# Kernel optimization log

Measured on AMD Instinct MI355X. Metric: run time of the kernel, lower is better.

## Reference

```python
import jax, jax.numpy as jnp
import numpy as np

NUM_QUBIT = 23
N0 = 2
DIM = 2 ** NUM_QUBIT  # 8388608


def setup_inputs() -> dict:
    key = jax.random.key(0)
    ks = jax.random.split(key, 6)
    shape = (N0, DIM)
    code0_real = jax.random.normal(ks[0], shape, jnp.float32)
    code0_imag = jax.random.normal(ks[1], shape, jnp.float32)
    code1_real = jax.random.normal(ks[2], shape, jnp.float32)
    code1_imag = jax.random.normal(ks[3], shape, jnp.float32)
    # per-qubit 2x2 unitaries: random complex matrices, unitarized via QR
    ur = jax.random.normal(ks[4], (NUM_QUBIT, 2, 2), jnp.float32)
    ui = jax.random.normal(ks[5], (NUM_QUBIT, 2, 2), jnp.float32)
    q, _ = jnp.linalg.qr(ur + 1j * ui)  # [n,2,2] complex64 unitary
    return {
        "code0_real": code0_real,
        "code0_imag": code0_imag,
        "code1_real": code1_real,
        "code1_imag": code1_imag,
        "unitary_real": jnp.real(q).astype(jnp.float32),
        "unitary_imag": jnp.imag(q).astype(jnp.float32),
    }


def reference(code0_real, code0_imag, code1_real, code1_imag,
              unitary_real, unitary_imag):
    code0 = code0_real + 1j * code0_imag            # [N0, 2^n] complex64
    code1 = code1_real + 1j * code1_imag            # [N0, 2^n]
    unitary = unitary_real + 1j * unitary_imag      # [n, 2, 2]
    n = unitary.shape[0]
    n0 = code0.shape[0]
    # sequential per-qubit 2x2 gate application on the statevectors
    for ind0 in range(n):
        tmp0 = code0.reshape(n0 * 2 ** ind0, 2, -1)  # [N0*2^i, 2, 2^(n-i-1)]
        # out[a,d,c] = sum_b tmp0[a,b,c] * U[b,d]
        code0 = jnp.einsum('abc,bd->adc', tmp0, unitary[ind0]).reshape(n0, -1)
    overlap = (jnp.conj(code0) @ code1.T).reshape(-1)  # [N0*N0]
    loss = n0 - jnp.real(jnp.vdot(overlap, overlap))
    return loss
```

## Files before the change

kernel.cpp:

```cpp
#include <hip/hip_runtime.h>

#define DIM_ (1 << 23)
#define N0_ 2

__device__ float g_acc[8];

__device__ __forceinline__ int swz(int x) {
    return x ^ ((x >> 5) & 3) ^ (((x >> 7) & 7) << 2);
}

__device__ __forceinline__ void gload(const float* __restrict__ ur,
                                      const float* __restrict__ ui, int q,
                                      float2& u00, float2& u01, float2& u10, float2& u11) {
    u00 = make_float2(ur[q * 4 + 0], ui[q * 4 + 0]);
    u01 = make_float2(ur[q * 4 + 1], ui[q * 4 + 1]);
    u10 = make_float2(ur[q * 4 + 2], ui[q * 4 + 2]);
    u11 = make_float2(ur[q * 4 + 3], ui[q * 4 + 3]);
}

__device__ __forceinline__ void bfly(float2& a0, float2& a1,
                                     float2 u00, float2 u01, float2 u10, float2 u11) {
    float2 n0, n1;
    n0.x = a0.x * u00.x - a0.y * u00.y + a1.x * u10.x - a1.y * u10.y;
    n0.y = a0.x * u00.y + a0.y * u00.x + a1.x * u10.y + a1.y * u10.x;
    n1.x = a0.x * u01.x - a0.y * u01.y + a1.x * u11.x - a1.y * u11.y;
    n1.y = a0.x * u01.y + a0.y * u01.x + a1.x * u11.y + a1.y * u11.x;
    a0 = n0; a1 = n1;
}

#define BFLY16(S, Q)                                                           \
    do {                                                                       \
        float2 u00, u01, u10, u11;                                             \
        gload(ur, ui, (Q), u00, u01, u10, u11);                                \
        _Pragma("unroll")                                                      \
        for (int m0 = 0; m0 < 16; ++m0)                                        \
            if (!(m0 & (S))) bfly(v[m0], v[m0 + (S)], u00, u01, u10, u11);     \
    } while (0)

template <bool INTER>
__global__ __launch_bounds__(512, 2) void k_low(
    const float* __restrict__ inr, const float* __restrict__ ini,
    const float* __restrict__ ur, const float* __restrict__ ui,
    float2* __restrict__ outI, float* __restrict__ outR, float* __restrict__ outJ) {
    __shared__ float2 buf[8192];
    const int t = threadIdx.x;
    const int H = blockIdx.x;
    const int base = blockIdx.y * DIM_ + (H << 13);

    float2 v[16];
#pragma unroll
    for (int k = 0; k < 4; ++k) {
        const int y = (k << 11) | (t << 2);
        const float4 re = *(const float4*)(inr + base + y);
        const float4 im = *(const float4*)(ini + base + y);
        v[k * 4 + 0] = make_float2(re.x, im.x);
        v[k * 4 + 1] = make_float2(re.y, im.y);
        v[k * 4 + 2] = make_float2(re.z, im.z);
        v[k * 4 + 3] = make_float2(re.w, im.w);
    }
    BFLY16(1, 22);
    BFLY16(2, 21);
    BFLY16(4, 11);
    BFLY16(8, 10);
#pragma unroll
    for (int m = 0; m < 16; ++m)
        buf[swz(((m >> 2) << 11) | (t << 2) | (m & 3))] = v[m];
    __syncthreads();
#pragma unroll
    for (int m = 0; m < 16; ++m)
        v[m] = buf[swz((t & 3) | (m << 2) | ((t >> 2) << 6))];
    BFLY16(1, 20);
    BFLY16(2, 19);
    BFLY16(4, 18);
    BFLY16(8, 17);
#pragma unroll
    for (int m = 0; m < 16; ++m)
        buf[swz((t & 3) | (m << 2) | ((t >> 2) << 6))] = v[m];
    __syncthreads();
#pragma unroll
    for (int m = 0; m < 16; ++m)
        v[m] = buf[swz((t & 63) | (m << 6) | ((t >> 6) << 10))];
    BFLY16(1, 16);
    BFLY16(2, 15);
    BFLY16(4, 14);
    BFLY16(8, 13);
#pragma unroll
    for (int m = 0; m < 16; ++m)
        buf[swz((t & 63) | (m << 6) | ((t >> 6) << 10))] = v[m];
    __syncthreads();
    {
        float2 u00, u01, u10, u11;
        gload(ur, ui, 12, u00, u01, u10, u11);
#pragma unroll
        for (int rp = 0; rp < 4; ++rp) {
            const int x0 = (rp << 11) | (t << 1);
            float2 a0 = buf[swz(x0)];
            float2 a1 = buf[swz(x0 | 1)];
            float2 b0 = buf[swz(x0 | 1024)];
            float2 b1 = buf[swz(x0 | 1025)];
            bfly(a0, b0, u00, u01, u10, u11);
            bfly(a1, b1, u00, u01, u10, u11);
            if (INTER) {
                const int l0 = x0, l1 = x0 | 1024;
                const int o0 = ((l0 >> 3) << 13) | (H << 3) | (l0 & 7);
                const int o1 = ((l1 >> 3) << 13) | (H << 3) | (l1 & 7);
                float2* p = outI + blockIdx.y * DIM_;
                *(float4*)(p + o0) = make_float4(a0.x, a0.y, a1.x, a1.y);
                *(float4*)(p + o1) = make_float4(b0.x, b0.y, b1.x, b1.y);
            } else {
                *(float2*)(outR + base + x0) = make_float2(a0.x, a1.x);
                *(float2*)(outJ + base + x0) = make_float2(a0.y, a1.y);
                *(float2*)(outR + base + (x0 | 1024)) = make_float2(b0.x, b1.x);
                *(float2*)(outJ + base + (x0 | 1024)) = make_float2(b0.y, b1.y);
            }
        }
    }
}

template <bool INTER>
__device__ __forceinline__ void high_pass(
    float2 (&v)[16], float2* buf, const int t, const int g, const int i,
    const float2* __restrict__ wsI, const float* __restrict__ wsR,
    const float* __restrict__ wsJ,
    const float* __restrict__ ur, const float* __restrict__ ui) {
    if constexpr (INTER) {
        const float4* wsv = (const float4*)(wsI + i * DIM_ + (g << 13));
#pragma unroll
        for (int k = 0; k < 4; ++k)
#pragma unroll
            for (int jh = 0; jh < 2; ++jh) {
                const float4 f = wsv[(k << 10) | (t << 1) | jh];
                v[k * 4 + jh * 2 + 0] = make_float2(f.x, f.y);
                v[k * 4 + jh * 2 + 1] = make_float2(f.z, f.w);
            }
    } else {
#pragma unroll
        for (int k = 0; k < 4; ++k) {
            const int y0 = (k << 11) | (t << 2);
            const int a = ((y0 >> 3) << 13) | (g << 3) | (y0 & 7);
            const float4 re = *(const float4*)(wsR + i * DIM_ + a);
            const float4 im = *(const float4*)(wsJ + i * DIM_ + a);
            v[k * 4 + 0] = make_float2(re.x, im.x);
            v[k * 4 + 1] = make_float2(re.y, im.y);
            v[k * 4 + 2] = make_float2(re.z, im.z);
            v[k * 4 + 3] = make_float2(re.w, im.w);
        }
    }
    BFLY16(4, 1);
    BFLY16(8, 0);
#pragma unroll
    for (int m = 0; m < 16; ++m)
        buf[swz(((m >> 2) << 11) | (t << 2) | (m & 3))] = v[m];
    __syncthreads();
#pragma unroll
    for (int m = 0; m < 16; ++m)
        v[m] = buf[swz((t & 7) | (m << 3) | ((t >> 3) << 7))];
    BFLY16(1, 9);
    BFLY16(2, 8);
    BFLY16(4, 7);
    BFLY16(8, 6);
#pragma unroll
    for (int m = 0; m < 16; ++m)
        buf[swz((t & 7) | (m << 3) | ((t >> 3) << 7))] = v[m];
    __syncthreads();
#pragma unroll
    for (int m = 0; m < 16; ++m)
        v[m] = buf[swz((t & 127) | (m << 7) | ((t >> 7) << 11))];
    BFLY16(1, 5);
    BFLY16(2, 4);
    BFLY16(4, 3);
    BFLY16(8, 2);
}

template <bool INTER>
__global__ __launch_bounds__(512, 2) void k_high(
    const float2* __restrict__ wsI, const float* __restrict__ wsR, const float* __restrict__ wsJ,
    const float* __restrict__ c1r, const float* __restrict__ c1i,
    const float* __restrict__ ur, const float* __restrict__ ui) {
    __shared__ float2 buf[8192];
    const int t = threadIdx.x;
    const int g = blockIdx.x;
    float acc[8];
#pragma unroll
    for (int k = 0; k < 8; ++k) acc[k] = 0.f;

    float2 v0[16], v1[16];
    high_pass<INTER>(v0, buf, t, g, 0, wsI, wsR, wsJ, ur, ui);
    __syncthreads();
    high_pass<INTER>(v1, buf, t, g, 1, wsI, wsR, wsJ, ur, ui);

#pragma unroll
    for (int m = 0; m < 16; ++m) {
        const int y = (t & 127) | (m << 7) | ((t >> 7) << 11);
        const int idx = ((y >> 3) << 13) | (g << 3) | (y & 7);
        const float ar = c1r[idx], ai = c1i[idx];
        const float br = c1r[DIM_ + idx], bi = c1i[DIM_ + idx];
        acc[0] += v0[m].x * ar + v0[m].y * ai;
        acc[1] += v0[m].x * ai - v0[m].y * ar;
        acc[2] += v0[m].x * br + v0[m].y * bi;
        acc[3] += v0[m].x * bi - v0[m].y * br;
        acc[4] += v1[m].x * ar + v1[m].y * ai;
        acc[5] += v1[m].x * ai - v1[m].y * ar;
        acc[6] += v1[m].x * br + v1[m].y * bi;
        acc[7] += v1[m].x * bi - v1[m].y * br;
    }

#pragma unroll
    for (int k = 0; k < 8; ++k)
#pragma unroll
        for (int off = 32; off > 0; off >>= 1)
            acc[k] += __shfl_down(acc[k], off, 64);
    __syncthreads();
    float* red = (float*)buf;
    const int wave = t >> 6, lane = t & 63;
    if (lane == 0) {
#pragma unroll
        for (int k = 0; k < 8; ++k) red[wave * 8 + k] = acc[k];
    }
    __syncthreads();
    if (t < 8) {
        float s = 0.f;
#pragma unroll
        for (int w = 0; w < 8; ++w) s += red[w * 8 + t];
        atomicAdd(&g_acc[t], s);
    }
}

__global__ void k_zero() {
    if (threadIdx.x < 8) g_acc[threadIdx.x] = 0.f;
}

__global__ void k_fin(float* __restrict__ out) {
    if (threadIdx.x == 0) {
        float s = 0.f;
#pragma unroll
        for (int k = 0; k < 4; ++k)
            s += g_acc[2 * k] * g_acc[2 * k] + g_acc[2 * k + 1] * g_acc[2 * k + 1];
        out[0] = (float)N0_ - s;
    }
}

extern "C" void kernel_launch(void* const* d_in, const int* in_sizes, int n_in,
                              void* d_out, int out_size, void* d_ws, size_t ws_size,
                              hipStream_t stream) {
    const float* c0r = (const float*)d_in[0];
    const float* c0i = (const float*)d_in[1];
    const float* c1r = (const float*)d_in[2];
    const float* c1i = (const float*)d_in[3];
    const float* ur  = (const float*)d_in[4];
    const float* ui  = (const float*)d_in[5];
    float* out = (float*)d_out;

    const size_t need = (size_t)N0_ * DIM_ * sizeof(float2);
    k_zero<<<1, 64, 0, stream>>>();
    dim3 g1(1024, N0_);
    if (d_ws != nullptr && ws_size >= need) {
        float2* wsI = (float2*)d_ws;
        k_low<true><<<g1, 512, 0, stream>>>(c0r, c0i, ur, ui, wsI, nullptr, nullptr);
        k_high<true><<<1024, 512, 0, stream>>>(wsI, nullptr, nullptr, c1r, c1i, ur, ui);
    } else {
        float* oR = (float*)c0r;
        float* oJ = (float*)c0i;
        k_low<false><<<g1, 512, 0, stream>>>(c0r, c0i, ur, ui, nullptr, oR, oJ);
        k_high<false><<<1024, 512, 0, stream>>>(nullptr, oR, oJ, c1r, c1i, ur, ui);
    }
    k_fin<<<1, 64, 0, stream>>>(out);
}
```

Before: 419.4 us.

## Rebalance qubit split between passes with smaller low-pass tiles and coalesced c1 loads

The low pass now handles 4096-element tiles with 256-thread blocks, twice as many blocks and half the shared memory. This moves qubit 10 from the low pass into the high pass, where it is applied after an extra shared-memory transpose. That transpose gives each thread 16 contiguous elements, so the overlap step reads code1 as float4 vectors instead of scattered scalars. The accumulator zeroing is folded into k_low, which removes one kernel launch. The cost is an extra LDS round trip and barrier in each high pass, plus a race risk: k_low's zeroing is ordered only by stream order ahead of k_high.

```diff
diff --git a/kernel.cpp b/kernel.cpp
--- a/kernel.cpp
+++ b/kernel.cpp
@@ -38,19 +38,22 @@
     } while (0)
 
 template <bool INTER>
-__global__ __launch_bounds__(512, 2) void k_low(
+__global__ __launch_bounds__(256, 5) void k_low(
     const float* __restrict__ inr, const float* __restrict__ ini,
     const float* __restrict__ ur, const float* __restrict__ ui,
     float2* __restrict__ outI, float* __restrict__ outR, float* __restrict__ outJ) {
-    __shared__ float2 buf[8192];
+    __shared__ float2 buf[4096];
     const int t = threadIdx.x;
-    const int H = blockIdx.x;
-    const int base = blockIdx.y * DIM_ + (H << 13);
+    const int C = blockIdx.x;
+    const int iv = blockIdx.y;
+    const int base = iv * DIM_ + (C << 12);
+
+    if (C == 0 && iv == 0 && t < 8) g_acc[t] = 0.f;
 
     float2 v[16];
 #pragma unroll
     for (int k = 0; k < 4; ++k) {
-        const int y = (k << 11) | (t << 2);
+        const int y = (k << 10) | (t << 2);
         const float4 re = *(const float4*)(inr + base + y);
         const float4 im = *(const float4*)(ini + base + y);
         v[k * 4 + 0] = make_float2(re.x, im.x);
@@ -60,11 +63,11 @@
     }
     BFLY16(1, 22);
     BFLY16(2, 21);
-    BFLY16(4, 11);
-    BFLY16(8, 10);
-#pragma unroll
-    for (int m = 0; m < 16; ++m)
-        buf[swz(((m >> 2) << 11) | (t << 2) | (m & 3))] = v[m];
+    BFLY16(4, 12);
+    BFLY16(8, 11);
+#pragma unroll
+    for (int m = 0; m < 16; ++m)
+        buf[swz(((m >> 2) << 10) | (t << 2) | (m & 3))] = v[m];
     __syncthreads();
 #pragma unroll
     for (int m = 0; m < 16; ++m)
@@ -88,43 +91,30 @@
     for (int m = 0; m < 16; ++m)
         buf[swz((t & 63) | (m << 6) | ((t >> 6) << 10))] = v[m];
     __syncthreads();
-    {
-        float2 u00, u01, u10, u11;
-        gload(ur, ui, 12, u00, u01, u10, u11);
-#pragma unroll
-        for (int rp = 0; rp < 4; ++rp) {
-            const int x0 = (rp << 11) | (t << 1);
-            float2 a0 = buf[swz(x0)];
-            float2 a1 = buf[swz(x0 | 1)];
-            float2 b0 = buf[swz(x0 | 1024)];
-            float2 b1 = buf[swz(x0 | 1025)];
-            bfly(a0, b0, u00, u01, u10, u11);
-            bfly(a1, b1, u00, u01, u10, u11);
-            if (INTER) {
-                const int l0 = x0, l1 = x0 | 1024;
-                const int o0 = ((l0 >> 3) << 13) | (H << 3) | (l0 & 7);
-                const int o1 = ((l1 >> 3) << 13) | (H << 3) | (l1 & 7);
-                float2* p = outI + blockIdx.y * DIM_;
-                *(float4*)(p + o0) = make_float4(a0.x, a0.y, a1.x, a1.y);
-                *(float4*)(p + o1) = make_float4(b0.x, b0.y, b1.x, b1.y);
-            } else {
-                *(float2*)(outR + base + x0) = make_float2(a0.x, a1.x);
-                *(float2*)(outJ + base + x0) = make_float2(a0.y, a1.y);
-                *(float2*)(outR + base + (x0 | 1024)) = make_float2(b0.x, b1.x);
-                *(float2*)(outJ + base + (x0 | 1024)) = make_float2(b0.y, b1.y);
-            }
+#pragma unroll
+    for (int r = 0; r < 8; ++r) {
+        const int l12 = (r << 9) | (t << 1);
+        const float2 a = buf[swz(l12)];
+        const float2 b = buf[swz(l12 | 1)];
+        if (INTER) {
+            const int o = ((l12 >> 2) << 13) | ((C >> 1) << 3) | ((C & 1) << 2) | (l12 & 3);
+            *(float4*)(outI + iv * DIM_ + o) = make_float4(a.x, a.y, b.x, b.y);
+        } else {
+            *(float2*)(outR + base + l12) = make_float2(a.x, b.x);
+            *(float2*)(outJ + base + l12) = make_float2(a.y, b.y);
         }
     }
 }
 
 template <bool INTER>
 __device__ __forceinline__ void high_pass(
-    float2 (&v)[16], float2* buf, const int t, const int g, const int i,
+    float2 (&d)[16], float2* buf, const int t, const int g, const int iv,
     const float2* __restrict__ wsI, const float* __restrict__ wsR,
     const float* __restrict__ wsJ,
     const float* __restrict__ ur, const float* __restrict__ ui) {
+    float2 v[16];
     if constexpr (INTER) {
-        const float4* wsv = (const float4*)(wsI + i * DIM_ + (g << 13));
+        const float4* wsv = (const float4*)(wsI + iv * DIM_ + (g << 13));
 #pragma unroll
         for (int k = 0; k < 4; ++k)
 #pragma unroll
@@ -136,10 +126,9 @@
     } else {
 #pragma unroll
         for (int k = 0; k < 4; ++k) {
-            const int y0 = (k << 11) | (t << 2);
-            const int a = ((y0 >> 3) << 13) | (g << 3) | (y0 & 7);
-            const float4 re = *(const float4*)(wsR + i * DIM_ + a);
-            const float4 im = *(const float4*)(wsJ + i * DIM_ + a);
+            const int a = (((k << 9) | t) << 12) | (g << 2);
+            const float4 re = *(const float4*)(wsR + iv * DIM_ + a);
+            const float4 im = *(const float4*)(wsJ + iv * DIM_ + a);
             v[k * 4 + 0] = make_float2(re.x, im.x);
             v[k * 4 + 1] = make_float2(re.y, im.y);
             v[k * 4 + 2] = make_float2(re.z, im.z);
@@ -170,6 +159,20 @@
     BFLY16(2, 4);
     BFLY16(4, 3);
     BFLY16(8, 2);
+#pragma unroll
+    for (int m = 0; m < 16; ++m)
+        buf[swz((t & 127) | (m << 7) | ((t >> 7) << 11))] = v[m];
+    __syncthreads();
+#pragma unroll
+    for (int j = 0; j < 16; ++j)
+        d[j] = buf[swz((t << 4) | j)];
+    {
+        float2 u00, u01, u10, u11;
+        gload(ur, ui, 10, u00, u01, u10, u11);
+#pragma unroll
+        for (int j = 0; j < 16; ++j)
+            if (!(j & 4)) bfly(d[j], d[j | 4], u00, u01, u10, u11);
+    }
 }
 
 template <bool INTER>
@@ -180,29 +183,36 @@
     __shared__ float2 buf[8192];
     const int t = threadIdx.x;
     const int g = blockIdx.x;
+
+    float2 d0[16], d1[16];
+    high_pass<INTER>(d0, buf, t, g, 0, wsI, wsR, wsJ, ur, ui);
+    __syncthreads();
+    high_pass<INTER>(d1, buf, t, g, 1, wsI, wsR, wsJ, ur, ui);
+
     float acc[8];
 #pragma unroll
     for (int k = 0; k < 8; ++k) acc[k] = 0.f;
-
-    float2 v0[16], v1[16];
-    high_pass<INTER>(v0, buf, t, g, 0, wsI, wsR, wsJ, ur, ui);
-    __syncthreads();
-    high_pass<INTER>(v1, buf, t, g, 1, wsI, wsR, wsJ, ur, ui);
-
-#pragma unroll
-    for (int m = 0; m < 16; ++m) {
-        const int y = (t & 127) | (m << 7) | ((t >> 7) << 11);
-        const int idx = ((y >> 3) << 13) | (g << 3) | (y & 7);
-        const float ar = c1r[idx], ai = c1i[idx];
-        const float br = c1r[DIM_ + idx], bi = c1i[DIM_ + idx];
-        acc[0] += v0[m].x * ar + v0[m].y * ai;
-        acc[1] += v0[m].x * ai - v0[m].y * ar;
-        acc[2] += v0[m].x * br + v0[m].y * bi;
-        acc[3] += v0[m].x * bi - v0[m].y * br;
-        acc[4] += v1[m].x * ar + v1[m].y * ai;
-        acc[5] += v1[m].x * ai - v1[m].y * ar;
-        acc[6] += v1[m].x * br + v1[m].y * bi;
-        acc[7] += v1[m].x * bi - v1[m].y * br;
+    const int col = g << 2;
+#pragma unroll
+    for (int jv = 0; jv < 2; ++jv) {
+        const float* __restrict__ pr = c1r + jv * DIM_;
+        const float* __restrict__ pi = c1i + jv * DIM_;
+#pragma unroll
+        for (int w = 0; w < 4; ++w) {
+            const int R = (t << 2) | w;
+            const float4 yr = *(const float4*)(pr + ((long long)R << 12) + col);
+            const float4 yi = *(const float4*)(pi + ((long long)R << 12) + col);
+#pragma unroll
+            for (int e = 0; e < 4; ++e) {
+                const int j = (w << 2) | e;
+                const float ar = ((const float*)&yr)[e];
+                const float ai = ((const float*)&yi)[e];
+                acc[jv * 2 + 0] += d0[j].x * ar + d0[j].y * ai;
+                acc[jv * 2 + 1] += d0[j].x * ai - d0[j].y * ar;
+                acc[jv * 2 + 4] += d1[j].x * ar + d1[j].y * ai;
+                acc[jv * 2 + 5] += d1[j].x * ai - d1[j].y * ar;
+            }
+        }
     }
 
 #pragma unroll
@@ -224,10 +234,6 @@
         for (int w = 0; w < 8; ++w) s += red[w * 8 + t];
         atomicAdd(&g_acc[t], s);
     }
-}
-
-__global__ void k_zero() {
-    if (threadIdx.x < 8) g_acc[threadIdx.x] = 0.f;
 }
 
 __global__ void k_fin(float* __restrict__ out) {
@@ -252,16 +258,15 @@
     float* out = (float*)d_out;
 
     const size_t need = (size_t)N0_ * DIM_ * sizeof(float2);
-    k_zero<<<1, 64, 0, stream>>>();
-    dim3 g1(1024, N0_);
+    dim3 g1(2048, N0_);
     if (d_ws != nullptr && ws_size >= need) {
         float2* wsI = (float2*)d_ws;
-        k_low<true><<<g1, 512, 0, stream>>>(c0r, c0i, ur, ui, wsI, nullptr, nullptr);
+        k_low<true><<<g1, 256, 0, stream>>>(c0r, c0i, ur, ui, wsI, nullptr, nullptr);
         k_high<true><<<1024, 512, 0, stream>>>(wsI, nullptr, nullptr, c1r, c1i, ur, ui);
     } else {
         float* oR = (float*)c0r;
         float* oJ = (float*)c0i;
-        k_low<false><<<g1, 512, 0, stream>>>(c0r, c0i, ur, ui, nullptr, oR, oJ);
+        k_low<false><<<g1, 256, 0, stream>>>(c0r, c0i, ur, ui, nullptr, oR, oJ);
         k_high<false><<<1024, 512, 0, stream>>>(nullptr, oR, oJ, c1r, c1i, ur, ui);
     }
     k_fin<<<1, 64, 0, stream>>>(out);
```

After: 512.7 us. 22.3% more time.
